# Kernel optimization log

Measured on AMD Instinct MI355X. Metric: run time of the kernel, lower is better.

## Reference

```python
import jax, jax.numpy as jnp
from jax import lax
import numpy as np

D_MODEL = 96; D_STATE = 16; SSM_RATIO = 2.0; D_CONV = 3; K = 4
D_INNER = int(SSM_RATIO * D_MODEL)      # 192
DT_RANK = -(-D_MODEL // 16)             # ceil(96/16) = 6
B_SZ = 4; H = 32; W = 32

# ---- zig-zag (snake) index helpers (static numpy) ----
def _snake_h(Hh, Ww):
    idx = np.tile(np.arange(Ww), (Hh, 1)); idx[1::2] = idx[1::2, ::-1]; return idx  # (H,W)

def _snake_v(Hh, Ww):
    idx = np.tile(np.arange(Hh)[:, None], (1, Ww)); idx[:, 1::2] = idx[::-1, 1::2]; return idx  # (H,W)

def _h_scan(x, d):
    Hh, Ww = x.shape[-2:]
    if d == 'left':
        x = jnp.flip(x, (-1, -2))
    return x[:, :, np.arange(Hh)[:, None], _snake_h(Hh, Ww)]

def _v_scan(x, d):
    Bb, Cc, Hh, Ww = x.shape
    if d == 'up':
        x = jnp.flip(x, (-1, -2))
    t = x[:, :, _snake_v(Hh, Ww), np.arange(Ww)[None, :]]  # gather along H per column
    return jnp.swapaxes(t, -1, -2).reshape(Bb, Cc, Hh, Ww)

def _h_merge(x, d):
    Hh, Ww = x.shape[-2:]
    t = x[:, :, np.arange(Hh)[:, None], _snake_h(Hh, Ww)]
    if d == 'left':
        t = jnp.flip(t, (-1, -2))
    return t

def _v_merge(x, d):
    Hh, Ww = x.shape[-2:]
    t2 = jnp.swapaxes(x, -1, -2)  # (B,C,W,H); requires H==W like the torch source
    t = t2[:, :, _snake_v(Hh, Ww), np.arange(Ww)[None, :]]
    if d == 'up':
        t = jnp.flip(t, (-1, -2))
    return t

def cross_scan(x):
    return jnp.stack([_v_scan(x, 'down'), _v_scan(x, 'up'), _h_scan(x, 'right'), _h_scan(x, 'left')], axis=1)

def cross_merge(ys):
    return (_v_merge(ys[:, 0], 'down') + _v_merge(ys[:, 1], 'up')
            + _h_merge(ys[:, 2], 'right') + _h_merge(ys[:, 3], 'left'))

def selective_scan(u, delta, A, Bs, Cs, Dp, delta_bias):
    # u,delta:(B,K,D,L)  A:(K,D,N)  Bs,Cs:(B,K,N,L)  Dp,delta_bias:(K,D)
    delta = jax.nn.softplus(delta + delta_bias[None, :, :, None])
    dA = jnp.exp(jnp.einsum('bkdl,kdn->lbkdn', delta, A))
    dBu = jnp.einsum('bkdl,bkdl,bknl->lbkdn', delta, u, Bs)
    Ct = jnp.moveaxis(Cs, -1, 0)  # (L,B,K,N)
    def step(h, inp):
        dA_t, dBu_t, c_t = inp
        h = dA_t * h + dBu_t
        return h, jnp.einsum('bkdn,bkn->bkd', h, c_t)
    h0 = jnp.zeros(dA.shape[1:], u.dtype)
    _, ys = lax.scan(step, h0, (dA, dBu, Ct))
    return jnp.moveaxis(ys, 0, -1) + Dp[None, :, :, None] * u  # (B,K,D,L)

def setup_inputs() -> dict:
    key = jax.random.key(0)
    ks = jax.random.split(key, 8)
    x = jax.random.normal(ks[0], (B_SZ, D_MODEL, H, W), jnp.float32)
    in_proj_w = jax.random.normal(ks[1], (2 * D_INNER, D_MODEL), jnp.float32) * (D_MODEL ** -0.5)
    conv_w = jax.random.normal(ks[2], (D_INNER, 1, D_CONV, D_CONV), jnp.float32) * 0.2  # depthwise
    conv_b = jnp.zeros((D_INNER,), jnp.float32)
    x_proj_w = jax.random.normal(ks[3], (K, DT_RANK + 2 * D_STATE, D_INNER), jnp.float32) * (D_INNER ** -0.5)
    s = DT_RANK ** -0.5
    dt_w = jax.random.uniform(ks[4], (K, D_INNER, DT_RANK), jnp.float32, -s, s)
    dt = jax.random.uniform(ks[5], (K, D_INNER), jnp.float32, 0.001, 0.1)
    dt_b = jnp.log(jnp.expm1(dt))  # inverse softplus, as in dt_init
    A_logs = jnp.tile(jnp.log(jnp.arange(1, D_STATE + 1, dtype=jnp.float32)), (K * D_INNER, 1))
    Ds = jnp.ones((K * D_INNER,), jnp.float32)
    gn_gamma = jnp.ones((D_INNER,), jnp.float32)
    gn_beta = jnp.zeros((D_INNER,), jnp.float32)
    out_proj_w = jax.random.normal(ks[6], (D_MODEL, D_INNER), jnp.float32) * (D_INNER ** -0.5)
    return {'x': x, 'in_proj_w': in_proj_w, 'conv_w': conv_w, 'conv_b': conv_b,
            'x_proj_w': x_proj_w, 'dt_w': dt_w, 'dt_b': dt_b, 'A_logs': A_logs, 'Ds': Ds,
            'gn_gamma': gn_gamma, 'gn_beta': gn_beta, 'out_proj_w': out_proj_w}

def reference(x, in_proj_w, conv_w, conv_b, x_proj_w, dt_w, dt_b, A_logs, Ds, gn_gamma, gn_beta, out_proj_w):
    Bb, _, Hh, Ww = x.shape; L = Hh * Ww
    xz = jnp.einsum('bchw,oc->bohw', x, in_proj_w)          # in_proj (1x1 conv, no bias)
    xx, z = jnp.split(xz, 2, axis=1)
    z = jax.nn.silu(z)
    xx = lax.conv_general_dilated(xx, conv_w, (1, 1), 'SAME', feature_group_count=D_INNER,
                                  dimension_numbers=('NCHW', 'OIHW', 'NCHW')) + conv_b[None, :, None, None]
    xx = jax.nn.silu(xx)
    xs = cross_scan(xx).reshape(Bb, K, D_INNER, L)          # 4-direction zig-zag scan
    x_dbl = jnp.einsum('bkdl,kcd->bkcl', xs, x_proj_w)
    dts = jnp.einsum('bkrl,kdr->bkdl', x_dbl[:, :, :DT_RANK], dt_w)
    Bs = x_dbl[:, :, DT_RANK:DT_RANK + D_STATE]
    Cs = x_dbl[:, :, DT_RANK + D_STATE:]
    A = -jnp.exp(A_logs).reshape(K, D_INNER, D_STATE)
    y = selective_scan(xs, dts, A, Bs, Cs, Ds.reshape(K, D_INNER), dt_b)
    y = cross_merge(y.reshape(Bb, K, D_INNER, Hh, Ww))       # (B,D,H,W)
    # out_norm: GroupNorm(1, d_inner) == layernorm over (C,H,W) per sample
    mu = jnp.mean(y, axis=(1, 2, 3), keepdims=True)
    var = jnp.var(y, axis=(1, 2, 3), keepdims=True)
    y = (y - mu) * lax.rsqrt(var + 1e-6)
    y = y * gn_gamma[None, :, None, None] + gn_beta[None, :, None, None]
    y = y * z
    return jnp.einsum('bchw,oc->bohw', y, out_proj_w)
```

## Files before the change

### kernel.cpp

```cpp
#include <hip/hip_runtime.h>
#include <math.h>

#define Bsz 4
#define DM 96
#define DI 192
#define NS 16
#define RK 6
#define KK 4
#define HH 32
#define WW 32
#define LL 1024
#define NC 32
#define CS 32

__device__ __forceinline__ float silu_f(float x) { return x / (1.f + __expf(-x)); }

__device__ __forceinline__ int hw_of_l(int k, int l) {
    int a = l >> 5, r = l & 31;
    int m = (a & 1) ? 31 - r : r;
    int h, w;
    if (k < 2) { w = a; h = m; }
    else       { h = a; w = m; }
    if (k & 1) { h = 31 - h; w = 31 - w; }
    return h * 32 + w;
}

__global__ void in_proj_k(const float* __restrict__ x, const float* __restrict__ w,
                          float* __restrict__ xx, float* __restrict__ zs,
                          float* __restrict__ stats) {
    int bi = blockIdx.x;
    int t = threadIdx.x;
    if (bi == 0 && t < 2 * Bsz) stats[t] = 0.f;
    int lb = bi & 3;
    int og = (bi >> 2) % 96;
    int b = bi / 384;
    int l = lb * 256 + t;
    const float* xb = x + (size_t)b * DM * LL + l;
    float acc[4];
#pragma unroll
    for (int g = 0; g < 4; g++) acc[g] = 0.f;
    for (int c = 0; c < DM; c++) {
        float xv = xb[(size_t)c * LL];
#pragma unroll
        for (int g = 0; g < 4; g++)
            acc[g] = fmaf(xv, w[(size_t)(og * 4 + g) * DM + c], acc[g]);
    }
#pragma unroll
    for (int g = 0; g < 4; g++) {
        int o = og * 4 + g;
        if (o < DI) xx[((size_t)b * DI + o) * LL + l] = acc[g];
        else        zs[((size_t)b * DI + (o - DI)) * LL + l] = silu_f(acc[g]);
    }
}

__global__ void convT_k(const float* __restrict__ xx, const float* __restrict__ cw,
                        const float* __restrict__ cb, float* __restrict__ xxT) {
    __shared__ float tile[32][33];
    int bi = blockIdx.x;
    int h0 = bi % 32;
    int dt = (bi / 32) % 6;
    int b = bi / 192;
    int d0 = dt * 32;
    int t = threadIdx.x;
    int wi = t & 31, dg = t >> 5;

#pragma unroll
    for (int pass = 0; pass < 4; pass++) {
        int di = pass * 8 + dg;
        int d = d0 + di;
        const float* xp = xx + ((size_t)b * DI + d) * LL;
        const float* wp = cw + d * 9;
        float acc = cb[d];
#pragma unroll
        for (int kh = 0; kh < 3; kh++) {
            int hh = h0 + kh - 1;
            if (hh < 0 || hh >= HH) continue;
#pragma unroll
            for (int kw = 0; kw < 3; kw++) {
                int ww2 = wi + kw - 1;
                if (ww2 < 0 || ww2 >= WW) continue;
                acc = fmaf(xp[hh * WW + ww2], wp[kh * 3 + kw], acc);
            }
        }
        tile[wi][di] = silu_f(acc);
    }
    __syncthreads();

    int di = t & 31, w8 = t >> 5;
#pragma unroll
    for (int rep = 0; rep < 4; rep++) {
        int w2 = rep * 8 + w8;
        xxT[((size_t)b * LL + h0 * 32 + w2) * DI + d0 + di] = tile[w2][di];
    }
}

__global__ void __launch_bounds__(512)
xdbl_k(const float* __restrict__ xxT, const float* __restrict__ xpw,
       float* __restrict__ xdbl) {
    __shared__ float tile[64 * 193];
    int blk = blockIdx.x;
    int bk = blk >> 4, lt = blk & 15;
    int k = bk & 3, b = bk >> 2;
    int t = threadIdx.x;

    const float* xb = xxT + (size_t)b * LL * DI;
#pragma unroll
    for (int i = 0; i < 6; i++) {
        int j4 = t + i * 512;
        int lr = j4 / 48;
        int d4 = j4 % 48;
        int hw = hw_of_l(k, lt * 64 + lr);
        float4 v = ((const float4*)(xb + (size_t)hw * DI))[d4];
        float* dst = &tile[lr * 193 + d4 * 4];
        dst[0] = v.x; dst[1] = v.y; dst[2] = v.z; dst[3] = v.w;
    }
    __syncthreads();

    int ll = t & 63;
    int cg = t >> 6;
    int c0 = cg * 5;
    int wlim = (c0 + 5 <= 38) ? 5 : (38 - c0);
    const float* wk = xpw + (size_t)k * 38 * DI;

    float acc[5];
#pragma unroll
    for (int j = 0; j < 5; j++) acc[j] = 0.f;
    const float* xrow = &tile[ll * 193];
#pragma unroll 4
    for (int d = 0; d < DI; d++) {
        float xv = xrow[d];
#pragma unroll
        for (int j = 0; j < 5; j++) {
            int cc = c0 + j; cc = (cc > 37) ? 37 : cc;
            acc[j] = fmaf(xv, wk[(size_t)cc * DI + d], acc[j]);
        }
    }
    float* orow = xdbl + ((size_t)bk * LL + lt * 64 + ll) * 38;
#pragma unroll
    for (int j = 0; j < 5; j++)
        if (j < wlim) orow[c0 + j] = acc[j];
}

#define XDP 40

__global__ void scan_p1(const float* __restrict__ xxT, const float* __restrict__ xdbl,
                        const float* __restrict__ dtw_g, const float* __restrict__ dtb_g,
                        const float* __restrict__ Alog,
                        float* __restrict__ Pst, float* __restrict__ Hloc) {
    __shared__ float u_tile[CS * 192];
    __shared__ float xd_tile[CS * XDP];
    int blk = blockIdx.x;
    int bk = blk / NC, c = blk % NC;
    int k = bk & 3, b = bk >> 2;
    int t = threadIdx.x;

    const float* xb = xxT + (size_t)b * LL * DI;
#pragma unroll
    for (int i = 0; i < 8; i++) {
        int j4 = t + i * 192;
        int s = j4 / 48, d4 = j4 % 48;
        int hw = hw_of_l(k, c * CS + s);
        float4 v = ((const float4*)(xb + (size_t)hw * DI))[d4];
        ((float4*)(&u_tile[s * 192]))[d4] = v;
    }
    const float* xdsrc = xdbl + ((size_t)bk * LL + c * CS) * 38;
    for (int i = t; i < CS * 38; i += 192) {
        int s = i / 38, j = i - s * 38;
        int pj = (j < 6) ? 32 + j : j - 6;
        xd_tile[s * XDP + pj] = xdsrc[i];
    }
    __syncthreads();

    int d = t;
    int kd = k * DI + d;
    float A0 = -__expf(Alog[(size_t)kd * NS]);
    bool pw = true;
#pragma unroll
    for (int n = 1; n < NS; n++) {
        float An = -__expf(Alog[(size_t)kd * NS + n]);
        pw = pw && (fabsf(An - (float)(n + 1) * A0) <= 1e-4f * (float)(n + 1));
    }
    float dtw[RK];
#pragma unroll
    for (int r = 0; r < RK; r++) dtw[r] = dtw_g[(size_t)kd * RK + r];
    float dtb = dtb_g[kd];

    float h[NS], P[NS];
#pragma unroll
    for (int n = 0; n < NS; n++) h[n] = 0.f;

    if (pw) {
        float R = 1.f;
        for (int s = 0; s < CS; s++) {
            const float4* xr = (const float4*)(&xd_tile[s * XDP]);
            float4 b0 = xr[0], b1 = xr[1], b2 = xr[2], b3 = xr[3];
            float4 q0 = xr[8], q1 = xr[9];
            float bb[16];
            bb[0]=b0.x; bb[1]=b0.y; bb[2]=b0.z; bb[3]=b0.w;
            bb[4]=b1.x; bb[5]=b1.y; bb[6]=b1.z; bb[7]=b1.w;
            bb[8]=b2.x; bb[9]=b2.y; bb[10]=b2.z; bb[11]=b2.w;
            bb[12]=b3.x; bb[13]=b3.y; bb[14]=b3.z; bb[15]=b3.w;
            float dt = dtb;
            dt = fmaf(q0.x, dtw[0], dt); dt = fmaf(q0.y, dtw[1], dt);
            dt = fmaf(q0.z, dtw[2], dt); dt = fmaf(q0.w, dtw[3], dt);
            dt = fmaf(q1.x, dtw[4], dt); dt = fmaf(q1.y, dtw[5], dt);
            dt = (dt > 20.f) ? dt : __logf(1.f + __expf(dt));
            float du = dt * u_tile[s * 192 + d];
            float r1 = __expf(dt * A0);
            float r2 = r1 * r1, r4 = r2 * r2, r8 = r4 * r4;
            float aa[16];
            aa[0] = r1; aa[1] = r2; aa[2] = r1 * r2; aa[3] = r4;
#pragma unroll
            for (int n = 0; n < 4; n++) aa[n + 4] = aa[n] * r4;
#pragma unroll
            for (int n = 0; n < 8; n++) aa[n + 8] = aa[n] * r8;
#pragma unroll
            for (int n = 0; n < NS; n++) h[n] = fmaf(aa[n], h[n], du * bb[n]);
            R *= r1;
        }
        float R2 = R * R, R4 = R2 * R2, R8 = R4 * R4;
        P[0] = R; P[1] = R2; P[2] = R * R2; P[3] = R4;
#pragma unroll
        for (int n = 0; n < 4; n++) P[n + 4] = P[n] * R4;
        P[7] = R8;
#pragma unroll
        for (int n = 0; n < 8; n++) P[n + 8] = P[n] * R8;
    } else {
        float A[NS];
#pragma unroll
        for (int n = 0; n < NS; n++) A[n] = -__expf(Alog[(size_t)kd * NS + n]);
#pragma unroll
        for (int n = 0; n < NS; n++) P[n] = 1.f;
        for (int s = 0; s < CS; s++) {
            const float4* xr = (const float4*)(&xd_tile[s * XDP]);
            float4 b0 = xr[0], b1 = xr[1], b2 = xr[2], b3 = xr[3];
            float4 q0 = xr[8], q1 = xr[9];
            float bb[16];
            bb[0]=b0.x; bb[1]=b0.y; bb[2]=b0.z; bb[3]=b0.w;
            bb[4]=b1.x; bb[5]=b1.y; bb[6]=b1.z; bb[7]=b1.w;
            bb[8]=b2.x; bb[9]=b2.y; bb[10]=b2.z; bb[11]=b2.w;
            bb[12]=b3.x; bb[13]=b3.y; bb[14]=b3.z; bb[15]=b3.w;
            float dt = dtb;
            dt = fmaf(q0.x, dtw[0], dt); dt = fmaf(q0.y, dtw[1], dt);
            dt = fmaf(q0.z, dtw[2], dt); dt = fmaf(q0.w, dtw[3], dt);
            dt = fmaf(q1.x, dtw[4], dt); dt = fmaf(q1.y, dtw[5], dt);
            dt = (dt > 20.f) ? dt : __logf(1.f + __expf(dt));
            float du = dt * u_tile[s * 192 + d];
#pragma unroll
            for (int n = 0; n < NS; n++) {
                float a = __expf(dt * A[n]);
                h[n] = fmaf(a, h[n], du * bb[n]);
                P[n] *= a;
            }
        }
    }
    if (c < NC - 1) {
        size_t base = ((size_t)blk * DI + d) * NS;
#pragma unroll
        for (int n = 0; n < NS; n++) { Pst[base + n] = P[n]; Hloc[base + n] = h[n]; }
    }
}

__global__ void scan_mid(const float* __restrict__ Pst, float* __restrict__ Hloc) {
    int gid = blockIdx.x * 256 + threadIdx.x;
    int bk = gid / 1536;
    int j = gid % 1536;
    const float2* Pp = (const float2*)(Pst + (size_t)bk * NC * (DI * NS)) + j;
    float2* Hp = (float2*)(Hloc + (size_t)bk * NC * (DI * NS)) + j;
    const int S = (DI * NS) / 2;

    float2 h = make_float2(0.f, 0.f);
    float2 P[4], L[4];
#pragma unroll
    for (int q = 0; q < 4; q++) { P[q] = Pp[(size_t)q * S]; L[q] = Hp[(size_t)q * S]; }
    for (int c = 0; c < NC; c += 4) {
        float2 Pn[4], Ln[4];
        if (c + 4 < NC) {
#pragma unroll
            for (int q = 0; q < 4; q++) {
                Pn[q] = Pp[(size_t)(c + 4 + q) * S];
                Ln[q] = Hp[(size_t)(c + 4 + q) * S];
            }
        }
#pragma unroll
        for (int q = 0; q < 4; q++) {
            Hp[(size_t)(c + q) * S] = h;
            h.x = fmaf(P[q].x, h.x, L[q].x);
            h.y = fmaf(P[q].y, h.y, L[q].y);
        }
#pragma unroll
        for (int q = 0; q < 4; q++) { P[q] = Pn[q]; L[q] = Ln[q]; }
    }
}

__global__ void scan_p3(const float* __restrict__ xxT, const float* __restrict__ xdbl,
                        const float* __restrict__ dtw_g, const float* __restrict__ dtb_g,
                        const float* __restrict__ Alog, const float* __restrict__ Ds,
                        const float* __restrict__ Hin, float* __restrict__ ysm) {
    __shared__ float u_tile[CS * 192];
    __shared__ float xd_tile[CS * XDP];
    int blk = blockIdx.x;
    int bk = blk / NC, c = blk % NC;
    int k = bk & 3, b = bk >> 2;
    int t = threadIdx.x;

    const float* xb = xxT + (size_t)b * LL * DI;
#pragma unroll
    for (int i = 0; i < 8; i++) {
        int j4 = t + i * 192;
        int s = j4 / 48, d4 = j4 % 48;
        int hw = hw_of_l(k, c * CS + s);
        float4 v = ((const float4*)(xb + (size_t)hw * DI))[d4];
        ((float4*)(&u_tile[s * 192]))[d4] = v;
    }
    const float* xdsrc = xdbl + ((size_t)bk * LL + c * CS) * 38;
    for (int i = t; i < CS * 38; i += 192) {
        int s = i / 38, j = i - s * 38;
        int pj = (j < 6) ? 32 + j : j - 6;
        xd_tile[s * XDP + pj] = xdsrc[i];
    }
    __syncthreads();

    int d = t;
    int kd = k * DI + d;
    float A0 = -__expf(Alog[(size_t)kd * NS]);
    bool pw = true;
#pragma unroll
    for (int n = 1; n < NS; n++) {
        float An = -__expf(Alog[(size_t)kd * NS + n]);
        pw = pw && (fabsf(An - (float)(n + 1) * A0) <= 1e-4f * (float)(n + 1));
    }
    float dtw[RK];
#pragma unroll
    for (int r = 0; r < RK; r++) dtw[r] = dtw_g[(size_t)kd * RK + r];
    float dtb = dtb_g[kd];
    float Dp = Ds[kd];

    float h[NS];
    size_t hbase = ((size_t)blk * DI + d) * NS;
#pragma unroll
    for (int n = 0; n < NS; n++) h[n] = Hin[hbase + n];

    float* yk = ysm + (size_t)bk * LL * DI;

    if (pw) {
        for (int s = 0; s < CS; s++) {
            const float4* xr = (const float4*)(&xd_tile[s * XDP]);
            float4 b0 = xr[0], b1 = xr[1], b2 = xr[2], b3 = xr[3];
            float4 c0 = xr[4], c1 = xr[5], c2 = xr[6], c3 = xr[7];
            float4 q0 = xr[8], q1 = xr[9];
            float bb[16], cc[16];
            bb[0]=b0.x; bb[1]=b0.y; bb[2]=b0.z; bb[3]=b0.w;
            bb[4]=b1.x; bb[5]=b1.y; bb[6]=b1.z; bb[7]=b1.w;
            bb[8]=b2.x; bb[9]=b2.y; bb[10]=b2.z; bb[11]=b2.w;
            bb[12]=b3.x; bb[13]=b3.y; bb[14]=b3.z; bb[15]=b3.w;
            cc[0]=c0.x; cc[1]=c0.y; cc[2]=c0.z; cc[3]=c0.w;
            cc[4]=c1.x; cc[5]=c1.y; cc[6]=c1.z; cc[7]=c1.w;
            cc[8]=c2.x; cc[9]=c2.y; cc[10]=c2.z; cc[11]=c2.w;
            cc[12]=c3.x; cc[13]=c3.y; cc[14]=c3.z; cc[15]=c3.w;
            float dt = dtb;
            dt = fmaf(q0.x, dtw[0], dt); dt = fmaf(q0.y, dtw[1], dt);
            dt = fmaf(q0.z, dtw[2], dt); dt = fmaf(q0.w, dtw[3], dt);
            dt = fmaf(q1.x, dtw[4], dt); dt = fmaf(q1.y, dtw[5], dt);
            dt = (dt > 20.f) ? dt : __logf(1.f + __expf(dt));
            float u = u_tile[s * 192 + d];
            float du = dt * u;
            float r1 = __expf(dt * A0);
            float r2 = r1 * r1, r4 = r2 * r2, r8 = r4 * r4;
            float aa[16];
            aa[0] = r1; aa[1] = r2; aa[2] = r1 * r2; aa[3] = r4;
#pragma unroll
            for (int n = 0; n < 4; n++) aa[n + 4] = aa[n] * r4;
#pragma unroll
            for (int n = 0; n < 8; n++) aa[n + 8] = aa[n] * r8;
            float y = 0.f;
#pragma unroll
            for (int n = 0; n < NS; n++) {
                h[n] = fmaf(aa[n], h[n], du * bb[n]);
                y = fmaf(h[n], cc[n], y);
            }
            int hw = hw_of_l(k, c * CS + s);
            yk[(size_t)hw * DI + d] = fmaf(Dp, u, y);
        }
    } else {
        float A[NS];
#pragma unroll
        for (int n = 0; n < NS; n++) A[n] = -__expf(Alog[(size_t)kd * NS + n]);
        for (int s = 0; s < CS; s++) {
            const float4* xr = (const float4*)(&xd_tile[s * XDP]);
            float4 b0 = xr[0], b1 = xr[1], b2 = xr[2], b3 = xr[3];
            float4 c0 = xr[4], c1 = xr[5], c2 = xr[6], c3 = xr[7];
            float4 q0 = xr[8], q1 = xr[9];
            float bb[16], cc[16];
            bb[0]=b0.x; bb[1]=b0.y; bb[2]=b0.z; bb[3]=b0.w;
            bb[4]=b1.x; bb[5]=b1.y; bb[6]=b1.z; bb[7]=b1.w;
            bb[8]=b2.x; bb[9]=b2.y; bb[10]=b2.z; bb[11]=b2.w;
            bb[12]=b3.x; bb[13]=b3.y; bb[14]=b3.z; bb[15]=b3.w;
            cc[0]=c0.x; cc[1]=c0.y; cc[2]=c0.z; cc[3]=c0.w;
            cc[4]=c1.x; cc[5]=c1.y; cc[6]=c1.z; cc[7]=c1.w;
            cc[8]=c2.x; cc[9]=c2.y; cc[10]=c2.z; cc[11]=c2.w;
            cc[12]=c3.x; cc[13]=c3.y; cc[14]=c3.z; cc[15]=c3.w;
            float dt = dtb;
            dt = fmaf(q0.x, dtw[0], dt); dt = fmaf(q0.y, dtw[1], dt);
            dt = fmaf(q0.z, dtw[2], dt); dt = fmaf(q0.w, dtw[3], dt);
            dt = fmaf(q1.x, dtw[4], dt); dt = fmaf(q1.y, dtw[5], dt);
            dt = (dt > 20.f) ? dt : __logf(1.f + __expf(dt));
            float u = u_tile[s * 192 + d];
            float du = dt * u;
            float y = 0.f;
#pragma unroll
            for (int n = 0; n < NS; n++) {
                float a = __expf(dt * A[n]);
                h[n] = fmaf(a, h[n], du * bb[n]);
                y = fmaf(h[n], cc[n], y);
            }
            int hw = hw_of_l(k, c * CS + s);
            yk[(size_t)hw * DI + d] = fmaf(Dp, u, y);
        }
    }
}

#define MT 8
__global__ void merge_k(const float* __restrict__ ysm, float* __restrict__ ym,
                        float* __restrict__ stats) {
    __shared__ float tile[MT][DI + 1];
    __shared__ float sh1[3], sh2[3];
    int b = blockIdx.y;
    int hw0 = blockIdx.x * MT;
    int d = threadIdx.x;
    const float* yb = ysm + (size_t)b * KK * LL * DI;

    float s1 = 0.f, s2 = 0.f;
#pragma unroll
    for (int hwi = 0; hwi < MT; hwi++) {
        int hw = hw0 + hwi;
        float v = yb[((size_t)0 * LL + hw) * DI + d]
                + yb[((size_t)1 * LL + hw) * DI + d]
                + yb[((size_t)2 * LL + hw) * DI + d]
                + yb[((size_t)3 * LL + hw) * DI + d];
        tile[hwi][d] = v;
        s1 += v; s2 = fmaf(v, v, s2);
    }
#pragma unroll
    for (int off = 32; off > 0; off >>= 1) {
        s1 += __shfl_down(s1, off);
        s2 += __shfl_down(s2, off);
    }
    int lane = threadIdx.x & 63, wid = threadIdx.x >> 6;
    if (lane == 0) { sh1[wid] = s1; sh2[wid] = s2; }
    __syncthreads();
    if (threadIdx.x == 0) {
        atomicAdd(&stats[b * 2],     sh1[0] + sh1[1] + sh1[2]);
        atomicAdd(&stats[b * 2 + 1], sh2[0] + sh2[1] + sh2[2]);
    }
#pragma unroll
    for (int rep = 0; rep < MT; rep++) {
        int j = rep * DI + threadIdx.x;
        int d2 = j >> 3;
        int hwi = j & (MT - 1);
        ym[((size_t)b * DI + d2) * LL + hw0 + hwi] = tile[hwi][d2];
    }
}

__global__ void outz_k(const float* __restrict__ ym, const float* __restrict__ zs,
                       const float* __restrict__ g, const float* __restrict__ be,
                       const float* __restrict__ stats, const float* __restrict__ wo,
                       float* __restrict__ out) {
    int bi = blockIdx.x;
    int t = threadIdx.x;
    int lb = bi & 3;
    int og = (bi >> 2) % 32;
    int b = bi / 128;
    int l = lb * 256 + t;

    const float Ninv = 1.f / (float)(DI * LL);
    float mu = stats[b * 2] * Ninv;
    float var = stats[b * 2 + 1] * Ninv - mu * mu;
    float rstd = rsqrtf(var + 1e-6f);

    const float* yb = ym + (size_t)b * DI * LL + l;
    const float* zb = zs + (size_t)b * DI * LL + l;
    float acc[3];
#pragma unroll
    for (int gg = 0; gg < 3; gg++) acc[gg] = 0.f;
    for (int c = 0; c < DI; c++) {
        float v = (yb[(size_t)c * LL] - mu) * rstd * g[c] + be[c];
        float yv = v * zb[(size_t)c * LL];
#pragma unroll
        for (int gg = 0; gg < 3; gg++)
            acc[gg] = fmaf(yv, wo[(size_t)(og * 3 + gg) * DI + c], acc[gg]);
    }
#pragma unroll
    for (int gg = 0; gg < 3; gg++)
        out[((size_t)b * DM + og * 3 + gg) * LL + l] = acc[gg];
}

extern "C" void kernel_launch(void* const* d_in, const int* in_sizes, int n_in,
                              void* d_out, int out_size, void* d_ws, size_t ws_size,
                              hipStream_t stream) {
    const float* x    = (const float*)d_in[0];
    const float* ipw  = (const float*)d_in[1];
    const float* cw   = (const float*)d_in[2];
    const float* cb   = (const float*)d_in[3];
    const float* xpw  = (const float*)d_in[4];
    const float* dtw  = (const float*)d_in[5];
    const float* dtb  = (const float*)d_in[6];
    const float* Alog = (const float*)d_in[7];
    const float* Ds   = (const float*)d_in[8];
    const float* gng  = (const float*)d_in[9];
    const float* gnb  = (const float*)d_in[10];
    const float* opw  = (const float*)d_in[11];
    float* out = (float*)d_out;

    float* ws = (float*)d_ws;
    const size_t o_xx   = 0;
    const size_t o_zs   = o_xx   + (size_t)Bsz * DI * LL;
    const size_t o_xxT  = o_zs   + (size_t)Bsz * DI * LL;
    const size_t o_xdbl = o_xxT  + (size_t)Bsz * LL * DI;
    const size_t o_P    = o_xdbl + (size_t)Bsz * KK * LL * 38;
    const size_t o_H    = o_P    + (size_t)Bsz * KK * NC * DI * NS;
    const size_t o_ysm  = o_H    + (size_t)Bsz * KK * NC * DI * NS;
    const size_t o_st   = o_ysm  + (size_t)Bsz * KK * LL * DI;

    float* xx    = ws + o_xx;
    float* zs    = ws + o_zs;
    float* xxT   = ws + o_xxT;
    float* xdbl  = ws + o_xdbl;
    float* Pst   = ws + o_P;
    float* Hst   = ws + o_H;
    float* ysm   = ws + o_ysm;
    float* stats = ws + o_st;
    float* ym = xx;

    hipLaunchKernelGGL(in_proj_k, dim3(1536), dim3(256), 0, stream, x, ipw, xx, zs, stats);
    hipLaunchKernelGGL(convT_k, dim3(768), dim3(256), 0, stream, xx, cw, cb, xxT);
    hipLaunchKernelGGL(xdbl_k, dim3(256), dim3(512), 0, stream, xxT, xpw, xdbl);
    hipLaunchKernelGGL(scan_p1, dim3(Bsz * KK * NC), dim3(192), 0, stream,
                       xxT, xdbl, dtw, dtb, Alog, Pst, Hst);
    hipLaunchKernelGGL(scan_mid, dim3(96), dim3(256), 0, stream, Pst, Hst);
    hipLaunchKernelGGL(scan_p3, dim3(Bsz * KK * NC), dim3(192), 0, stream,
                       xxT, xdbl, dtw, dtb, Alog, Ds, Hst, ysm);
    hipLaunchKernelGGL(merge_k, dim3(LL / MT, Bsz), dim3(192), 0, stream, ysm, ym, stats);
    hipLaunchKernelGGL(outz_k, dim3(512), dim3(256), 0, stream, ym, zs, gng, gnb, stats, opw, out);
}
```

Baseline: 190.1 us.

## Fuse chunked scan phases into one single-pass decoupled-lookback kernel

Replaces the three-kernel chunked selective scan (local pass, sequential carry pass, recompute pass) with one kernel. Each block takes a dynamic chunk id from an atomic counter, publishes its local decay and state, then looks back through predecessor flags to build its incoming state. It publishes the inclusive state and runs the output pass from the tiles already in shared memory, caching dt in a new shared tile so it is not recomputed. This removes two launches and the re-reading of inputs, at the cost of spin-waiting, extra shared memory that may lower occupancy, and a third state buffer.

```diff
diff --git a/kernel.cpp b/kernel.cpp
--- a/kernel.cpp
+++ b/kernel.cpp
@@ -27,10 +27,13 @@
 
 __global__ void in_proj_k(const float* __restrict__ x, const float* __restrict__ w,
                           float* __restrict__ xx, float* __restrict__ zs,
-                          float* __restrict__ stats) {
+                          float* __restrict__ stats, int* __restrict__ flags) {
     int bi = blockIdx.x;
     int t = threadIdx.x;
-    if (bi == 0 && t < 2 * Bsz) stats[t] = 0.f;
+    if (bi == 0) {
+        if (t < 2 * Bsz) stats[t] = 0.f;
+        for (int i = t; i < 513; i += 256) flags[i] = 0;
+    }
     int lb = bi & 3;
     int og = (bi >> 2) % 96;
     int b = bi / 384;
@@ -143,16 +146,24 @@
 
 #define XDP 40
 
-__global__ void scan_p1(const float* __restrict__ xxT, const float* __restrict__ xdbl,
-                        const float* __restrict__ dtw_g, const float* __restrict__ dtb_g,
-                        const float* __restrict__ Alog,
-                        float* __restrict__ Pst, float* __restrict__ Hloc) {
+__global__ void __launch_bounds__(192)
+scan_sp(const float* __restrict__ xxT, const float* __restrict__ xdbl,
+        const float* __restrict__ dtw_g, const float* __restrict__ dtb_g,
+        const float* __restrict__ Alog, const float* __restrict__ Ds,
+        float* __restrict__ Ploc, float* __restrict__ Hloc,
+        float* __restrict__ Hinc, int* __restrict__ flags,
+        float* __restrict__ ysm) {
     __shared__ float u_tile[CS * 192];
     __shared__ float xd_tile[CS * XDP];
-    int blk = blockIdx.x;
+    __shared__ float dt_tile[CS * 192];
+    __shared__ int s_blk, s_flag;
+
+    int t = threadIdx.x;
+    if (t == 0) s_blk = atomicAdd(&flags[512], 1);
+    __syncthreads();
+    int blk = s_blk;
     int bk = blk / NC, c = blk % NC;
     int k = bk & 3, b = bk >> 2;
-    int t = threadIdx.x;
 
     const float* xb = xxT + (size_t)b * LL * DI;
 #pragma unroll
@@ -184,6 +195,7 @@
 #pragma unroll
     for (int r = 0; r < RK; r++) dtw[r] = dtw_g[(size_t)kd * RK + r];
     float dtb = dtb_g[kd];
+    float Dp = Ds[kd];
 
     float h[NS], P[NS];
 #pragma unroll
@@ -205,6 +217,7 @@
             dt = fmaf(q0.z, dtw[2], dt); dt = fmaf(q0.w, dtw[3], dt);
             dt = fmaf(q1.x, dtw[4], dt); dt = fmaf(q1.y, dtw[5], dt);
             dt = (dt > 20.f) ? dt : __logf(1.f + __expf(dt));
+            dt_tile[s * 192 + d] = dt;
             float du = dt * u_tile[s * 192 + d];
             float r1 = __expf(dt * A0);
             float r2 = r1 * r1, r4 = r2 * r2, r8 = r4 * r4;
@@ -245,6 +258,7 @@
             dt = fmaf(q0.z, dtw[2], dt); dt = fmaf(q0.w, dtw[3], dt);
             dt = fmaf(q1.x, dtw[4], dt); dt = fmaf(q1.y, dtw[5], dt);
             dt = (dt > 20.f) ? dt : __logf(1.f + __expf(dt));
+            dt_tile[s * 192 + d] = dt;
             float du = dt * u_tile[s * 192 + d];
 #pragma unroll
             for (int n = 0; n < NS; n++) {
@@ -254,93 +268,64 @@
             }
         }
     }
+
+    size_t pb = (size_t)blk * (NS * DI);
     if (c < NC - 1) {
-        size_t base = ((size_t)blk * DI + d) * NS;
-#pragma unroll
-        for (int n = 0; n < NS; n++) { Pst[base + n] = P[n]; Hloc[base + n] = h[n]; }
-    }
-}
-
-__global__ void scan_mid(const float* __restrict__ Pst, float* __restrict__ Hloc) {
-    int gid = blockIdx.x * 256 + threadIdx.x;
-    int bk = gid / 1536;
-    int j = gid % 1536;
-    const float2* Pp = (const float2*)(Pst + (size_t)bk * NC * (DI * NS)) + j;
-    float2* Hp = (float2*)(Hloc + (size_t)bk * NC * (DI * NS)) + j;
-    const int S = (DI * NS) / 2;
-
-    float2 h = make_float2(0.f, 0.f);
-    float2 P[4], L[4];
-#pragma unroll
-    for (int q = 0; q < 4; q++) { P[q] = Pp[(size_t)q * S]; L[q] = Hp[(size_t)q * S]; }
-    for (int c = 0; c < NC; c += 4) {
-        float2 Pn[4], Ln[4];
-        if (c + 4 < NC) {
-#pragma unroll
-            for (int q = 0; q < 4; q++) {
-                Pn[q] = Pp[(size_t)(c + 4 + q) * S];
-                Ln[q] = Hp[(size_t)(c + 4 + q) * S];
+#pragma unroll
+        for (int n = 0; n < NS; n++) {
+            Ploc[pb + n * DI + d] = P[n];
+            Hloc[pb + n * DI + d] = h[n];
+        }
+        __threadfence();
+        __syncthreads();
+        if (t == 0)
+            __hip_atomic_store(&flags[blk], 1, __ATOMIC_RELEASE, __HIP_MEMORY_SCOPE_AGENT);
+    }
+
+    float E[NS], Pa[NS];
+#pragma unroll
+    for (int n = 0; n < NS; n++) { E[n] = 0.f; Pa[n] = 1.f; }
+    int cc = c - 1;
+    while (cc >= 0) {
+        int fblk = bk * NC + cc;
+        if (t == 0) {
+            int f;
+            while ((f = __hip_atomic_load(&flags[fblk], __ATOMIC_ACQUIRE,
+                                          __HIP_MEMORY_SCOPE_AGENT)) == 0)
+                __builtin_amdgcn_s_sleep(8);
+            s_flag = f;
+        }
+        __syncthreads();
+        int f = s_flag;
+        __syncthreads();
+        size_t qb = (size_t)fblk * (NS * DI);
+        if (f == 2) {
+#pragma unroll
+            for (int n = 0; n < NS; n++)
+                E[n] = fmaf(Pa[n], Hinc[qb + n * DI + d], E[n]);
+            break;
+        } else {
+#pragma unroll
+            for (int n = 0; n < NS; n++) {
+                E[n] = fmaf(Pa[n], Hloc[qb + n * DI + d], E[n]);
+                Pa[n] *= Ploc[qb + n * DI + d];
             }
-        }
-#pragma unroll
-        for (int q = 0; q < 4; q++) {
-            Hp[(size_t)(c + q) * S] = h;
-            h.x = fmaf(P[q].x, h.x, L[q].x);
-            h.y = fmaf(P[q].y, h.y, L[q].y);
-        }
-#pragma unroll
-        for (int q = 0; q < 4; q++) { P[q] = Pn[q]; L[q] = Ln[q]; }
-    }
-}
-
-__global__ void scan_p3(const float* __restrict__ xxT, const float* __restrict__ xdbl,
-                        const float* __restrict__ dtw_g, const float* __restrict__ dtb_g,
-                        const float* __restrict__ Alog, const float* __restrict__ Ds,
-                        const float* __restrict__ Hin, float* __restrict__ ysm) {
-    __shared__ float u_tile[CS * 192];
-    __shared__ float xd_tile[CS * XDP];
-    int blk = blockIdx.x;
-    int bk = blk / NC, c = blk % NC;
-    int k = bk & 3, b = bk >> 2;
-    int t = threadIdx.x;
-
-    const float* xb = xxT + (size_t)b * LL * DI;
-#pragma unroll
-    for (int i = 0; i < 8; i++) {
-        int j4 = t + i * 192;
-        int s = j4 / 48, d4 = j4 % 48;
-        int hw = hw_of_l(k, c * CS + s);
-        float4 v = ((const float4*)(xb + (size_t)hw * DI))[d4];
-        ((float4*)(&u_tile[s * 192]))[d4] = v;
-    }
-    const float* xdsrc = xdbl + ((size_t)bk * LL + c * CS) * 38;
-    for (int i = t; i < CS * 38; i += 192) {
-        int s = i / 38, j = i - s * 38;
-        int pj = (j < 6) ? 32 + j : j - 6;
-        xd_tile[s * XDP + pj] = xdsrc[i];
-    }
-    __syncthreads();
-
-    int d = t;
-    int kd = k * DI + d;
-    float A0 = -__expf(Alog[(size_t)kd * NS]);
-    bool pw = true;
-#pragma unroll
-    for (int n = 1; n < NS; n++) {
-        float An = -__expf(Alog[(size_t)kd * NS + n]);
-        pw = pw && (fabsf(An - (float)(n + 1) * A0) <= 1e-4f * (float)(n + 1));
-    }
-    float dtw[RK];
-#pragma unroll
-    for (int r = 0; r < RK; r++) dtw[r] = dtw_g[(size_t)kd * RK + r];
-    float dtb = dtb_g[kd];
-    float Dp = Ds[kd];
-
-    float h[NS];
-    size_t hbase = ((size_t)blk * DI + d) * NS;
-#pragma unroll
-    for (int n = 0; n < NS; n++) h[n] = Hin[hbase + n];
-
+            cc--;
+        }
+    }
+
+    if (c < NC - 1) {
+#pragma unroll
+        for (int n = 0; n < NS; n++)
+            Hinc[pb + n * DI + d] = fmaf(P[n], E[n], h[n]);
+        __threadfence();
+        __syncthreads();
+        if (t == 0)
+            __hip_atomic_store(&flags[blk], 2, __ATOMIC_RELEASE, __HIP_MEMORY_SCOPE_AGENT);
+    }
+
+#pragma unroll
+    for (int n = 0; n < NS; n++) h[n] = E[n];
     float* yk = ysm + (size_t)bk * LL * DI;
 
     if (pw) {
@@ -348,21 +333,16 @@
             const float4* xr = (const float4*)(&xd_tile[s * XDP]);
             float4 b0 = xr[0], b1 = xr[1], b2 = xr[2], b3 = xr[3];
             float4 c0 = xr[4], c1 = xr[5], c2 = xr[6], c3 = xr[7];
-            float4 q0 = xr[8], q1 = xr[9];
-            float bb[16], cc[16];
+            float bb[16], cf[16];
             bb[0]=b0.x; bb[1]=b0.y; bb[2]=b0.z; bb[3]=b0.w;
             bb[4]=b1.x; bb[5]=b1.y; bb[6]=b1.z; bb[7]=b1.w;
             bb[8]=b2.x; bb[9]=b2.y; bb[10]=b2.z; bb[11]=b2.w;
             bb[12]=b3.x; bb[13]=b3.y; bb[14]=b3.z; bb[15]=b3.w;
-            cc[0]=c0.x; cc[1]=c0.y; cc[2]=c0.z; cc[3]=c0.w;
-            cc[4]=c1.x; cc[5]=c1.y; cc[6]=c1.z; cc[7]=c1.w;
-            cc[8]=c2.x; cc[9]=c2.y; cc[10]=c2.z; cc[11]=c2.w;
-            cc[12]=c3.x; cc[13]=c3.y; cc[14]=c3.z; cc[15]=c3.w;
-            float dt = dtb;
-            dt = fmaf(q0.x, dtw[0], dt); dt = fmaf(q0.y, dtw[1], dt);
-            dt = fmaf(q0.z, dtw[2], dt); dt = fmaf(q0.w, dtw[3], dt);
-            dt = fmaf(q1.x, dtw[4], dt); dt = fmaf(q1.y, dtw[5], dt);
-            dt = (dt > 20.f) ? dt : __logf(1.f + __expf(dt));
+            cf[0]=c0.x; cf[1]=c0.y; cf[2]=c0.z; cf[3]=c0.w;
+            cf[4]=c1.x; cf[5]=c1.y; cf[6]=c1.z; cf[7]=c1.w;
+            cf[8]=c2.x; cf[9]=c2.y; cf[10]=c2.z; cf[11]=c2.w;
+            cf[12]=c3.x; cf[13]=c3.y; cf[14]=c3.z; cf[15]=c3.w;
+            float dt = dt_tile[s * 192 + d];
             float u = u_tile[s * 192 + d];
             float du = dt * u;
             float r1 = __expf(dt * A0);
@@ -377,7 +357,7 @@
 #pragma unroll
             for (int n = 0; n < NS; n++) {
                 h[n] = fmaf(aa[n], h[n], du * bb[n]);
-                y = fmaf(h[n], cc[n], y);
+                y = fmaf(h[n], cf[n], y);
             }
             int hw = hw_of_l(k, c * CS + s);
             yk[(size_t)hw * DI + d] = fmaf(Dp, u, y);
@@ -390,21 +370,16 @@
             const float4* xr = (const float4*)(&xd_tile[s * XDP]);
             float4 b0 = xr[0], b1 = xr[1], b2 = xr[2], b3 = xr[3];
             float4 c0 = xr[4], c1 = xr[5], c2 = xr[6], c3 = xr[7];
-            float4 q0 = xr[8], q1 = xr[9];
-            float bb[16], cc[16];
+            float bb[16], cf[16];
             bb[0]=b0.x; bb[1]=b0.y; bb[2]=b0.z; bb[3]=b0.w;
             bb[4]=b1.x; bb[5]=b1.y; bb[6]=b1.z; bb[7]=b1.w;
             bb[8]=b2.x; bb[9]=b2.y; bb[10]=b2.z; bb[11]=b2.w;
             bb[12]=b3.x; bb[13]=b3.y; bb[14]=b3.z; bb[15]=b3.w;
-            cc[0]=c0.x; cc[1]=c0.y; cc[2]=c0.z; cc[3]=c0.w;
-            cc[4]=c1.x; cc[5]=c1.y; cc[6]=c1.z; cc[7]=c1.w;
-            cc[8]=c2.x; cc[9]=c2.y; cc[10]=c2.z; cc[11]=c2.w;
-            cc[12]=c3.x; cc[13]=c3.y; cc[14]=c3.z; cc[15]=c3.w;
-            float dt = dtb;
-            dt = fmaf(q0.x, dtw[0], dt); dt = fmaf(q0.y, dtw[1], dt);
-            dt = fmaf(q0.z, dtw[2], dt); dt = fmaf(q0.w, dtw[3], dt);
-            dt = fmaf(q1.x, dtw[4], dt); dt = fmaf(q1.y, dtw[5], dt);
-            dt = (dt > 20.f) ? dt : __logf(1.f + __expf(dt));
+            cf[0]=c0.x; cf[1]=c0.y; cf[2]=c0.z; cf[3]=c0.w;
+            cf[4]=c1.x; cf[5]=c1.y; cf[6]=c1.z; cf[7]=c1.w;
+            cf[8]=c2.x; cf[9]=c2.y; cf[10]=c2.z; cf[11]=c2.w;
+            cf[12]=c3.x; cf[13]=c3.y; cf[14]=c3.z; cf[15]=c3.w;
+            float dt = dt_tile[s * 192 + d];
             float u = u_tile[s * 192 + d];
             float du = dt * u;
             float y = 0.f;
@@ -412,7 +387,7 @@
             for (int n = 0; n < NS; n++) {
                 float a = __expf(dt * A[n]);
                 h[n] = fmaf(a, h[n], du * bb[n]);
-                y = fmaf(h[n], cc[n], y);
+                y = fmaf(h[n], cf[n], y);
             }
             int hw = hw_of_l(k, c * CS + s);
             yk[(size_t)hw * DI + d] = fmaf(Dp, u, y);
@@ -513,33 +488,35 @@
     float* out = (float*)d_out;
 
     float* ws = (float*)d_ws;
+    const size_t NPH  = (size_t)Bsz * KK * NC * DI * NS;
     const size_t o_xx   = 0;
     const size_t o_zs   = o_xx   + (size_t)Bsz * DI * LL;
     const size_t o_xxT  = o_zs   + (size_t)Bsz * DI * LL;
     const size_t o_xdbl = o_xxT  + (size_t)Bsz * LL * DI;
     const size_t o_P    = o_xdbl + (size_t)Bsz * KK * LL * 38;
-    const size_t o_H    = o_P    + (size_t)Bsz * KK * NC * DI * NS;
-    const size_t o_ysm  = o_H    + (size_t)Bsz * KK * NC * DI * NS;
+    const size_t o_H    = o_P    + NPH;
+    const size_t o_Hi   = o_H    + NPH;
+    const size_t o_ysm  = o_Hi   + NPH;
     const size_t o_st   = o_ysm  + (size_t)Bsz * KK * LL * DI;
+    const size_t o_fl   = o_st   + 16;
 
     float* xx    = ws + o_xx;
     float* zs    = ws + o_zs;
     float* xxT   = ws + o_xxT;
     float* xdbl  = ws + o_xdbl;
-    float* Pst   = ws + o_P;
-    float* Hst   = ws + o_H;
+    float* Ploc  = ws + o_P;
+    float* Hloc  = ws + o_H;
+    float* Hinc  = ws + o_Hi;
     float* ysm   = ws + o_ysm;
     float* stats = ws + o_st;
+    int*   flags = (int*)(ws + o_fl);
     float* ym = xx;
 
-    hipLaunchKernelGGL(in_proj_k, dim3(1536), dim3(256), 0, stream, x, ipw, xx, zs, stats);
+    hipLaunchKernelGGL(in_proj_k, dim3(1536), dim3(256), 0, stream, x, ipw, xx, zs, stats, flags);
     hipLaunchKernelGGL(convT_k, dim3(768), dim3(256), 0, stream, xx, cw, cb, xxT);
     hipLaunchKernelGGL(xdbl_k, dim3(256), dim3(512), 0, stream, xxT, xpw, xdbl);
-    hipLaunchKernelGGL(scan_p1, dim3(Bsz * KK * NC), dim3(192), 0, stream,
-                       xxT, xdbl, dtw, dtb, Alog, Pst, Hst);
-    hipLaunchKernelGGL(scan_mid, dim3(96), dim3(256), 0, stream, Pst, Hst);
-    hipLaunchKernelGGL(scan_p3, dim3(Bsz * KK * NC), dim3(192), 0, stream,
-                       xxT, xdbl, dtw, dtb, Alog, Ds, Hst, ysm);
+    hipLaunchKernelGGL(scan_sp, dim3(Bsz * KK * NC), dim3(192), 0, stream,
+                       xxT, xdbl, dtw, dtb, Alog, Ds, Ploc, Hloc, Hinc, flags, ysm);
     hipLaunchKernelGGL(merge_k, dim3(LL / MT, Bsz), dim3(192), 0, stream, ysm, ym, stats);
     hipLaunchKernelGGL(outz_k, dim3(512), dim3(256), 0, stream, ym, zs, gng, gnb, stats, opw, out);
 }
```

Result: slower. 325.9 us (+71.5%).

## Fuse chunk-carry propagation into scan output pass and halve xdbl tile size

Applied to the files above, without the earlier changes.

The separate scan_mid kernel that serially propagated chunk carries is removed. Each scan_p23 block now recomputes its incoming state by folding the (P, Hloc) summaries of all preceding chunks, which saves a launch and a global round trip. The summary layout is transposed to n-major with d contiguous so these loads coalesce. xdbl_k is also retiled to 32-row tiles with 3 outputs per thread over twice as many blocks, for more parallelism. The trade-off is redundant carry work, quadratic in chunk count, done by later chunks.

```diff
diff --git a/kernel.cpp b/kernel.cpp
--- a/kernel.cpp
+++ b/kernel.cpp
@@ -97,47 +97,47 @@
 __global__ void __launch_bounds__(512)
 xdbl_k(const float* __restrict__ xxT, const float* __restrict__ xpw,
        float* __restrict__ xdbl) {
-    __shared__ float tile[64 * 193];
+    __shared__ float tile[32 * 193];
     int blk = blockIdx.x;
-    int bk = blk >> 4, lt = blk & 15;
+    int bk = blk >> 5, lt = blk & 31;
     int k = bk & 3, b = bk >> 2;
     int t = threadIdx.x;
 
     const float* xb = xxT + (size_t)b * LL * DI;
 #pragma unroll
-    for (int i = 0; i < 6; i++) {
+    for (int i = 0; i < 3; i++) {
         int j4 = t + i * 512;
         int lr = j4 / 48;
         int d4 = j4 % 48;
-        int hw = hw_of_l(k, lt * 64 + lr);
+        int hw = hw_of_l(k, lt * 32 + lr);
         float4 v = ((const float4*)(xb + (size_t)hw * DI))[d4];
         float* dst = &tile[lr * 193 + d4 * 4];
         dst[0] = v.x; dst[1] = v.y; dst[2] = v.z; dst[3] = v.w;
     }
     __syncthreads();
 
-    int ll = t & 63;
-    int cg = t >> 6;
-    int c0 = cg * 5;
-    int wlim = (c0 + 5 <= 38) ? 5 : (38 - c0);
+    int ll = t & 31;
+    int cg = t >> 5;
+    int c0 = cg * 3;
+    int wlim = (c0 < 38) ? ((c0 + 3 <= 38) ? 3 : (38 - c0)) : 0;
     const float* wk = xpw + (size_t)k * 38 * DI;
 
-    float acc[5];
-#pragma unroll
-    for (int j = 0; j < 5; j++) acc[j] = 0.f;
+    float acc[3];
+#pragma unroll
+    for (int j = 0; j < 3; j++) acc[j] = 0.f;
     const float* xrow = &tile[ll * 193];
 #pragma unroll 4
     for (int d = 0; d < DI; d++) {
         float xv = xrow[d];
 #pragma unroll
-        for (int j = 0; j < 5; j++) {
+        for (int j = 0; j < 3; j++) {
             int cc = c0 + j; cc = (cc > 37) ? 37 : cc;
             acc[j] = fmaf(xv, wk[(size_t)cc * DI + d], acc[j]);
         }
     }
-    float* orow = xdbl + ((size_t)bk * LL + lt * 64 + ll) * 38;
-#pragma unroll
-    for (int j = 0; j < 5; j++)
+    float* orow = xdbl + ((size_t)bk * LL + lt * 32 + ll) * 38;
+#pragma unroll
+    for (int j = 0; j < 3; j++)
         if (j < wlim) orow[c0 + j] = acc[j];
 }
 
@@ -255,48 +255,20 @@
         }
     }
     if (c < NC - 1) {
-        size_t base = ((size_t)blk * DI + d) * NS;
-#pragma unroll
-        for (int n = 0; n < NS; n++) { Pst[base + n] = P[n]; Hloc[base + n] = h[n]; }
-    }
-}
-
-__global__ void scan_mid(const float* __restrict__ Pst, float* __restrict__ Hloc) {
-    int gid = blockIdx.x * 256 + threadIdx.x;
-    int bk = gid / 1536;
-    int j = gid % 1536;
-    const float2* Pp = (const float2*)(Pst + (size_t)bk * NC * (DI * NS)) + j;
-    float2* Hp = (float2*)(Hloc + (size_t)bk * NC * (DI * NS)) + j;
-    const int S = (DI * NS) / 2;
-
-    float2 h = make_float2(0.f, 0.f);
-    float2 P[4], L[4];
-#pragma unroll
-    for (int q = 0; q < 4; q++) { P[q] = Pp[(size_t)q * S]; L[q] = Hp[(size_t)q * S]; }
-    for (int c = 0; c < NC; c += 4) {
-        float2 Pn[4], Ln[4];
-        if (c + 4 < NC) {
-#pragma unroll
-            for (int q = 0; q < 4; q++) {
-                Pn[q] = Pp[(size_t)(c + 4 + q) * S];
-                Ln[q] = Hp[(size_t)(c + 4 + q) * S];
-            }
-        }
-#pragma unroll
-        for (int q = 0; q < 4; q++) {
-            Hp[(size_t)(c + q) * S] = h;
-            h.x = fmaf(P[q].x, h.x, L[q].x);
-            h.y = fmaf(P[q].y, h.y, L[q].y);
-        }
-#pragma unroll
-        for (int q = 0; q < 4; q++) { P[q] = Pn[q]; L[q] = Ln[q]; }
-    }
-}
-
-__global__ void scan_p3(const float* __restrict__ xxT, const float* __restrict__ xdbl,
-                        const float* __restrict__ dtw_g, const float* __restrict__ dtb_g,
-                        const float* __restrict__ Alog, const float* __restrict__ Ds,
-                        const float* __restrict__ Hin, float* __restrict__ ysm) {
+        size_t base = (size_t)blk * NS * DI + d;
+#pragma unroll
+        for (int n = 0; n < NS; n++) {
+            Pst[base + n * DI] = P[n];
+            Hloc[base + n * DI] = h[n];
+        }
+    }
+}
+
+__global__ void scan_p23(const float* __restrict__ xxT, const float* __restrict__ xdbl,
+                         const float* __restrict__ dtw_g, const float* __restrict__ dtb_g,
+                         const float* __restrict__ Alog, const float* __restrict__ Ds,
+                         const float* __restrict__ Pst, const float* __restrict__ Hloc,
+                         float* __restrict__ ysm) {
     __shared__ float u_tile[CS * 192];
     __shared__ float xd_tile[CS * XDP];
     int blk = blockIdx.x;
@@ -337,9 +309,17 @@
     float Dp = Ds[kd];
 
     float h[NS];
-    size_t hbase = ((size_t)blk * DI + d) * NS;
-#pragma unroll
-    for (int n = 0; n < NS; n++) h[n] = Hin[hbase + n];
+#pragma unroll
+    for (int n = 0; n < NS; n++) h[n] = 0.f;
+    for (int cc = 0; cc < c; cc++) {
+        size_t qb = (size_t)(bk * NC + cc) * NS * DI + d;
+#pragma unroll
+        for (int n = 0; n < NS; n++) {
+            float p  = Pst[qb + n * DI];
+            float hl = Hloc[qb + n * DI];
+            h[n] = fmaf(p, h[n], hl);
+        }
+    }
 
     float* yk = ysm + (size_t)bk * LL * DI;
 
@@ -349,15 +329,15 @@
             float4 b0 = xr[0], b1 = xr[1], b2 = xr[2], b3 = xr[3];
             float4 c0 = xr[4], c1 = xr[5], c2 = xr[6], c3 = xr[7];
             float4 q0 = xr[8], q1 = xr[9];
-            float bb[16], cc[16];
+            float bb[16], cf[16];
             bb[0]=b0.x; bb[1]=b0.y; bb[2]=b0.z; bb[3]=b0.w;
             bb[4]=b1.x; bb[5]=b1.y; bb[6]=b1.z; bb[7]=b1.w;
             bb[8]=b2.x; bb[9]=b2.y; bb[10]=b2.z; bb[11]=b2.w;
             bb[12]=b3.x; bb[13]=b3.y; bb[14]=b3.z; bb[15]=b3.w;
-            cc[0]=c0.x; cc[1]=c0.y; cc[2]=c0.z; cc[3]=c0.w;
-            cc[4]=c1.x; cc[5]=c1.y; cc[6]=c1.z; cc[7]=c1.w;
-            cc[8]=c2.x; cc[9]=c2.y; cc[10]=c2.z; cc[11]=c2.w;
-            cc[12]=c3.x; cc[13]=c3.y; cc[14]=c3.z; cc[15]=c3.w;
+            cf[0]=c0.x; cf[1]=c0.y; cf[2]=c0.z; cf[3]=c0.w;
+            cf[4]=c1.x; cf[5]=c1.y; cf[6]=c1.z; cf[7]=c1.w;
+            cf[8]=c2.x; cf[9]=c2.y; cf[10]=c2.z; cf[11]=c2.w;
+            cf[12]=c3.x; cf[13]=c3.y; cf[14]=c3.z; cf[15]=c3.w;
             float dt = dtb;
             dt = fmaf(q0.x, dtw[0], dt); dt = fmaf(q0.y, dtw[1], dt);
             dt = fmaf(q0.z, dtw[2], dt); dt = fmaf(q0.w, dtw[3], dt);
@@ -377,7 +357,7 @@
 #pragma unroll
             for (int n = 0; n < NS; n++) {
                 h[n] = fmaf(aa[n], h[n], du * bb[n]);
-                y = fmaf(h[n], cc[n], y);
+                y = fmaf(h[n], cf[n], y);
             }
             int hw = hw_of_l(k, c * CS + s);
             yk[(size_t)hw * DI + d] = fmaf(Dp, u, y);
@@ -391,15 +371,15 @@
             float4 b0 = xr[0], b1 = xr[1], b2 = xr[2], b3 = xr[3];
             float4 c0 = xr[4], c1 = xr[5], c2 = xr[6], c3 = xr[7];
             float4 q0 = xr[8], q1 = xr[9];
-            float bb[16], cc[16];
+            float bb[16], cf[16];
             bb[0]=b0.x; bb[1]=b0.y; bb[2]=b0.z; bb[3]=b0.w;
             bb[4]=b1.x; bb[5]=b1.y; bb[6]=b1.z; bb[7]=b1.w;
             bb[8]=b2.x; bb[9]=b2.y; bb[10]=b2.z; bb[11]=b2.w;
             bb[12]=b3.x; bb[13]=b3.y; bb[14]=b3.z; bb[15]=b3.w;
-            cc[0]=c0.x; cc[1]=c0.y; cc[2]=c0.z; cc[3]=c0.w;
-            cc[4]=c1.x; cc[5]=c1.y; cc[6]=c1.z; cc[7]=c1.w;
-            cc[8]=c2.x; cc[9]=c2.y; cc[10]=c2.z; cc[11]=c2.w;
-            cc[12]=c3.x; cc[13]=c3.y; cc[14]=c3.z; cc[15]=c3.w;
+            cf[0]=c0.x; cf[1]=c0.y; cf[2]=c0.z; cf[3]=c0.w;
+            cf[4]=c1.x; cf[5]=c1.y; cf[6]=c1.z; cf[7]=c1.w;
+            cf[8]=c2.x; cf[9]=c2.y; cf[10]=c2.z; cf[11]=c2.w;
+            cf[12]=c3.x; cf[13]=c3.y; cf[14]=c3.z; cf[15]=c3.w;
             float dt = dtb;
             dt = fmaf(q0.x, dtw[0], dt); dt = fmaf(q0.y, dtw[1], dt);
             dt = fmaf(q0.z, dtw[2], dt); dt = fmaf(q0.w, dtw[3], dt);
@@ -412,7 +392,7 @@
             for (int n = 0; n < NS; n++) {
                 float a = __expf(dt * A[n]);
                 h[n] = fmaf(a, h[n], du * bb[n]);
-                y = fmaf(h[n], cc[n], y);
+                y = fmaf(h[n], cf[n], y);
             }
             int hw = hw_of_l(k, c * CS + s);
             yk[(size_t)hw * DI + d] = fmaf(Dp, u, y);
@@ -513,13 +493,14 @@
     float* out = (float*)d_out;
 
     float* ws = (float*)d_ws;
+    const size_t NPH  = (size_t)Bsz * KK * NC * DI * NS;
     const size_t o_xx   = 0;
     const size_t o_zs   = o_xx   + (size_t)Bsz * DI * LL;
     const size_t o_xxT  = o_zs   + (size_t)Bsz * DI * LL;
     const size_t o_xdbl = o_xxT  + (size_t)Bsz * LL * DI;
     const size_t o_P    = o_xdbl + (size_t)Bsz * KK * LL * 38;
-    const size_t o_H    = o_P    + (size_t)Bsz * KK * NC * DI * NS;
-    const size_t o_ysm  = o_H    + (size_t)Bsz * KK * NC * DI * NS;
+    const size_t o_H    = o_P    + NPH;
+    const size_t o_ysm  = o_H    + NPH;
     const size_t o_st   = o_ysm  + (size_t)Bsz * KK * LL * DI;
 
     float* xx    = ws + o_xx;
@@ -534,12 +515,11 @@
 
     hipLaunchKernelGGL(in_proj_k, dim3(1536), dim3(256), 0, stream, x, ipw, xx, zs, stats);
     hipLaunchKernelGGL(convT_k, dim3(768), dim3(256), 0, stream, xx, cw, cb, xxT);
-    hipLaunchKernelGGL(xdbl_k, dim3(256), dim3(512), 0, stream, xxT, xpw, xdbl);
+    hipLaunchKernelGGL(xdbl_k, dim3(512), dim3(512), 0, stream, xxT, xpw, xdbl);
     hipLaunchKernelGGL(scan_p1, dim3(Bsz * KK * NC), dim3(192), 0, stream,
                        xxT, xdbl, dtw, dtb, Alog, Pst, Hst);
-    hipLaunchKernelGGL(scan_mid, dim3(96), dim3(256), 0, stream, Pst, Hst);
-    hipLaunchKernelGGL(scan_p3, dim3(Bsz * KK * NC), dim3(192), 0, stream,
-                       xxT, xdbl, dtw, dtb, Alog, Ds, Hst, ysm);
+    hipLaunchKernelGGL(scan_p23, dim3(Bsz * KK * NC), dim3(192), 0, stream,
+                       xxT, xdbl, dtw, dtb, Alog, Ds, Pst, Hst, ysm);
     hipLaunchKernelGGL(merge_k, dim3(LL / MT, Bsz), dim3(192), 0, stream, ysm, ym, stats);
     hipLaunchKernelGGL(outz_k, dim3(512), dim3(256), 0, stream, ym, zs, gng, gnb, stats, opw, out);
 }
```

Result: slower. 252.1 us (+32.6%).
